# Performance work log

Hardware: AMD Instinct MI355X
Metric: run time of the kernel (lower is better)

## Reference

```python
import jax, jax.numpy as jnp
import numpy as np

N_E = 8192      # codebook size
E_DIM = 256     # codebook dim
BETA = 0.25

def setup_inputs() -> dict:
    key = jax.random.key(0)
    k1, k2 = jax.random.split(key)
    z = jax.random.normal(k1, (4, E_DIM, 16, 16, 16), dtype=jnp.float32)
    weight = jax.random.normal(k2, (N_E, E_DIM), dtype=jnp.float32)
    return {"z": z, "weight": weight}

def reference(z, weight):
    # b c d h w -> b d h w c
    z_t = jnp.transpose(z, (0, 2, 3, 4, 1))
    zf = z_t.reshape(-1, E_DIM)                          # [N, e_dim]
    # l2 pairwise distances: |z|^2 + |w|^2 - 2 z.w^T
    d = (jnp.sum(zf * zf, axis=1, keepdims=True)
         + jnp.sum(weight * weight, axis=1)
         - 2.0 * jnp.einsum('bd,nd->bn', zf, weight))    # [N, n_e]
    idx = jnp.argmin(d, axis=1)                          # [N]
    z_q = weight[idx].reshape(z_t.shape)                 # gather lookup
    # perplexity from cluster assignment histogram (avoids dense one-hot)
    counts = jax.ops.segment_sum(jnp.ones_like(idx, dtype=z.dtype), idx,
                                 num_segments=N_E)
    avg_probs = counts / zf.shape[0]
    perplexity = jnp.exp(-jnp.sum(avg_probs * jnp.log(avg_probs + 1e-10)))
    # commitment loss (z_q detached)
    loss = BETA * jnp.mean((jax.lax.stop_gradient(z_q) - z_t) ** 2)
    # straight-through estimator
    z_q_st = z_t + jax.lax.stop_gradient(z_q - z_t)
    out = jnp.transpose(z_q_st, (0, 4, 1, 2, 3))         # b d h w c -> b c d h w
    return out, loss, perplexity, idx
```

## Files before the change

kernel.cpp:

```cpp
#include <hip/hip_runtime.h>
#include <stdint.h>


#define M_TOTAL 16384
#define N_CODES 8192
#define KDIM    256
#define SPATIAL 4096
#define NSPLIT  8
#define CODES_PER_SPLIT  1024
#define CHUNK_CODES      16
#define CHUNKS_PER_SPLIT 64
#define CHUNK_BYTES      9216
#define CHUNK_HALFS      4608

typedef _Float16 v8hf __attribute__((ext_vector_type(8)));
typedef _Float16 v4hf __attribute__((ext_vector_type(4)));
typedef float    v4f  __attribute__((ext_vector_type(4)));

#define WAITCNT_VM9   0x0F79
#define WAITCNT_VM0   0x0F70
#define WAITCNT_LGKM0 0xC07F

__global__ __launch_bounds__(256) void prep_w_kernel(
    const float* __restrict__ w, _Float16* __restrict__ wpk,
    int* __restrict__ counts, double* __restrict__ loss_acc)
{
    const int t = threadIdx.x;
    const int n = blockIdx.x * 4 + (t >> 6);
    const int lane = t & 63;
    v4f v = ((const v4f*)(w + (size_t)n * KDIM))[lane];
    v4hf hv;
    float s = 0.0f;
#pragma unroll
    for (int j = 0; j < 4; j++) {
        float f = v[j];
        s += f * f;
        hv[j] = (_Float16)f;
    }
    const int chunk = n >> 4;
    const int row   = n & 15;
    const int g     = lane >> 1;
    const int gg    = g ^ (n & 7);
    size_t off = (size_t)chunk * CHUNK_HALFS + row * 256 + gg * 8 + (lane & 1) * 4;
    *(v4hf*)(wpk + off) = hv;
#pragma unroll
    for (int o = 32; o >= 1; o >>= 1) s += __shfl_xor(s, o);
    if (lane == 0) {
        float* hwp = (float*)((char*)wpk + (size_t)chunk * CHUNK_BYTES + 8192);
        hwp[row] = 1024.0f - 0.5f * s;
    }
    const int gi = blockIdx.x * 256 + t;
    if (gi < N_CODES) counts[gi] = 0;
    if (gi == 0) *loss_acc = 0.0;
}

__device__ __forceinline__ void top2max_merge(uint32_t& v1, int& i1, uint32_t& v2, int& i2,
                                              uint32_t o1, int oi1, uint32_t o2, int oi2) {
    bool ob = (o1 > v1) || (o1 == v1 && oi1 < i1);
    uint32_t n1v, n2v; int n1i, n2i;
    if (ob) {
        bool t2 = (v1 > o2) || (v1 == o2 && i1 < oi2);
        n1v = o1; n1i = oi1;
        n2v = t2 ? v1 : o2; n2i = t2 ? i1 : oi2;
    } else {
        bool t2 = (o1 > v2) || (o1 == v2 && oi1 < i2);
        n1v = v1; n1i = i1;
        n2v = t2 ? o1 : v2; n2i = t2 ? oi1 : i2;
    }
    v1 = n1v; i1 = n1i; v2 = n2v; i2 = n2i;
}

__global__ __launch_bounds__(64, 2) void gemm_kernel(
    const float* __restrict__ z,
    const _Float16* __restrict__ wpk,
    int4* __restrict__ candbuf)
{
    __shared__ __align__(16) _Float16 lds[2][CHUNK_HALFS];

    const int bid   = blockIdx.x;
    const int split = bid & 7;
    const int rb    = bid >> 3;
    const int i0    = rb * 64;
    const int b     = i0 >> 12;
    const int s0    = i0 & (SPATIAL - 1);
    const int lane  = threadIdx.x;
    const int r     = lane & 15;
    const int q     = lane >> 4;

    const char* wsplit = (const char*)wpk + (size_t)split * CHUNKS_PER_SPLIT * CHUNK_BYTES;
    auto stage = [&](int chunk, int buf) {
        const char* gb = wsplit + (size_t)chunk * CHUNK_BYTES + lane * 16;
        _Float16* lb = &lds[buf][lane * 8];
#pragma unroll
        for (int j = 0; j < 9; j++) {
            __builtin_amdgcn_global_load_lds(
                (const __attribute__((address_space(1))) void*)(gb + j * 1024),
                (__attribute__((address_space(3))) void*)(lb + j * 512), 16, 0, 0);
        }
    };
    stage(0, 0);
    stage(1, 1);

    v8hf a[4][8];
    {
        const float* zb = z + ((size_t)b << 20) + (size_t)(s0 + r);
#pragma unroll
        for (int mt = 0; mt < 4; mt++) {
#pragma unroll
            for (int ks = 0; ks < 8; ks++) {
                const int kbase = ks * 32 + q * 8;
#pragma unroll
                for (int j = 0; j < 8; j++)
                    a[mt][ks][j] = (_Float16)zb[((size_t)(kbase + j) << 12) + mt * 16];
            }
        }
    }

    uint32_t k1[4][4], k2[4][4];
#pragma unroll
    for (int mt = 0; mt < 4; mt++)
#pragma unroll
    for (int g = 0; g < 4; g++) { k1[mt][g] = 0u; k2[mt][g] = 0u; }

    const int swz = r & 7;

    auto body = [&](int it, int buf) {
        const float hwv = *(const float*)((const char*)&lds[buf][0] + 8192 + r * 4);
        v4f acc[4];
#pragma unroll
        for (int mt = 0; mt < 4; mt++) acc[mt] = (v4f){hwv, hwv, hwv, hwv};

        const _Float16* L = &lds[buf][0];
#pragma unroll
        for (int ks = 0; ks < 8; ks++) {
            const int gran = ((ks << 2) | q) ^ swz;
            v8hf bh = *(const v8hf*)(L + r * 256 + (gran << 3));
#pragma unroll
            for (int mt = 0; mt < 4; mt++)
                acc[mt] = __builtin_amdgcn_mfma_f32_16x16x32_f16(a[mt][ks], bh, acc[mt], 0, 0, 0);
        }
        const uint32_t tag = (uint32_t)it;
#pragma unroll
        for (int mt = 0; mt < 4; mt++)
#pragma unroll
        for (int g = 0; g < 4; g++) {
            uint32_t key = (__float_as_uint(acc[mt][g]) & 0xFFFFFFC0u) | tag;
            uint32_t o1 = k1[mt][g], o2 = k2[mt][g];
            uint32_t hi = key > o2 ? key : o2;
            k2[mt][g] = hi < o1 ? hi : o1;
            k1[mt][g] = key > o1 ? key : o1;
        }
    };

#pragma unroll 1
    for (int it = 0; it < CHUNKS_PER_SPLIT - 1; it++) {
        const int buf = it & 1;
        __builtin_amdgcn_s_waitcnt(WAITCNT_VM9);
        body(it, buf);
        __builtin_amdgcn_s_waitcnt(WAITCNT_LGKM0);
        if (it < CHUNKS_PER_SPLIT - 2) stage(it + 2, buf);
    }
    __builtin_amdgcn_s_waitcnt(WAITCNT_VM0);
    body(CHUNKS_PER_SPLIT - 1, (CHUNKS_PER_SPLIT - 1) & 1);

    const int nsbase = split * CODES_PER_SPLIT + r;
#pragma unroll
    for (int mt = 0; mt < 4; mt++) {
#pragma unroll
        for (int g = 0; g < 4; g++) {
            uint32_t K1 = k1[mt][g], K2 = k2[mt][g];
            int n1 = nsbase + (int)((K1 & 63u) << 4);
            int n2 = nsbase + (int)((K2 & 63u) << 4);
#pragma unroll
            for (int off = 1; off < 16; off <<= 1) {
                uint32_t o1 = __shfl_xor(K1, off);
                int     on1 = __shfl_xor(n1, off);
                uint32_t o2 = __shfl_xor(K2, off);
                int     on2 = __shfl_xor(n2, off);
                top2max_merge(K1, n1, K2, n2, o1, on1, o2, on2);
            }
            if (r == 0) {
                const int row = i0 + mt * 16 + q * 4 + g;
                candbuf[(size_t)row * 8 + split] = make_int4((int)K1, n1, (int)K2, n2);
            }
        }
    }
}

__global__ __launch_bounds__(256) void finish_kernel(
    const float* __restrict__ z, const float* __restrict__ weight,
    const int4* __restrict__ candbuf,
    int* __restrict__ counts, double* __restrict__ loss_acc,
    float* __restrict__ out, float* __restrict__ out_idx_f)
{
    __shared__ int4  s_cand[32][8];
    __shared__ float s_zw[32][KDIM + 1];
    __shared__ int   s_fi[32];
    __shared__ double s_loss[4];

    const int i0 = blockIdx.x * 32;
    const int b  = i0 >> 12;
    const int s0 = i0 & (SPATIAL - 1);
    const int t  = threadIdx.x;

    s_cand[t >> 3][t & 7] = candbuf[(size_t)(i0 + (t >> 3)) * 8 + (t & 7)];

    for (int e = t; e < 32 * KDIM; e += 256) {
        const int c = e >> 5, rr = e & 31;
        s_zw[rr][c] = z[((size_t)b << 20) + ((size_t)c << 12) + s0 + rr];
    }
    __syncthreads();

    const int row = t >> 3, seg = t & 7;
    float zs[32];
#pragma unroll
    for (int j = 0; j < 32; j++) zs[j] = s_zw[row][seg * 32 + j];

    float da[16];
    float dmin_a = 3.4e38f;
#pragma unroll
    for (int sp = 0; sp < 8; sp++) {
        int4 c = s_cand[row][sp];
        da[sp * 2]     = 2048.0f - 2.0f * __uint_as_float((uint32_t)c.x & 0xFFFFFFC0u);
        da[sp * 2 + 1] = 2048.0f - 2.0f * __uint_as_float((uint32_t)c.z & 0xFFFFFFC0u);
        dmin_a = fminf(dmin_a, fminf(da[sp * 2], da[sp * 2 + 1]));
    }
    const float cutoff = dmin_a + 0.5f;

    double dbest = 1e300; int nbest = 0x7fffffff;
#pragma unroll 1
    for (int c = 0; c < 16; c++) {
        if (da[c] > cutoff) continue;
        int4 cc = s_cand[row][c >> 1];
        const int n = (c & 1) ? cc.w : cc.y;
        const float* wr = weight + (size_t)n * KDIM + seg * 32;
        double d = 0.0;
#pragma unroll
        for (int j = 0; j < 32; j++) {
            double df = (double)zs[j] - (double)wr[j];
            d += df * df;
        }
#pragma unroll
        for (int o = 1; o < 8; o <<= 1) d += __shfl_xor(d, o);
        if (d < dbest || (d == dbest && n < nbest)) { dbest = d; nbest = n; }
    }

    double lsum = 0.0;
    if (seg == 0) {
        s_fi[row] = nbest;
        out_idx_f[i0 + row] = (float)nbest;
        atomicAdd(&counts[nbest], 1);
        lsum = dbest;
    }
#pragma unroll
    for (int o = 1; o < 64; o <<= 1) lsum += __shfl_xor(lsum, o);
    if ((t & 63) == 0) s_loss[t >> 6] = lsum;
    __syncthreads();
    if (t == 0) atomicAdd(loss_acc, s_loss[0] + s_loss[1] + s_loss[2] + s_loss[3]);

    for (int e = t; e < 32 * KDIM; e += 256) {
        const int rr = e >> 8, c = e & 255;
        s_zw[rr][c] = weight[(size_t)s_fi[rr] * KDIM + c];
    }
    __syncthreads();
    const int m = t & 31, c0 = t >> 5;
    const size_t obase = ((size_t)b << 20) + (size_t)(s0 + m);
    for (int c = c0; c < KDIM; c += 8)
        out[obase + ((size_t)c << 12)] = s_zw[m][c];
}

__global__ void finalize_kernel(const int* __restrict__ counts,
                                const double* __restrict__ loss_acc,
                                float* __restrict__ out_scalars)
{
    const int t = threadIdx.x;
    double s = 0.0;
    for (int n = t; n < N_CODES; n += 256) {
        double p = (double)counts[n] / (double)M_TOTAL;
        s -= p * log(p + 1e-10);
    }
#pragma unroll
    for (int o = 32; o >= 1; o >>= 1) s += __shfl_xor(s, o);
    __shared__ double sds[4];
    if ((t & 63) == 0) sds[t >> 6] = s;
    __syncthreads();
    if (t == 0) {
        double tot = sds[0] + sds[1] + sds[2] + sds[3];
        out_scalars[0] = (float)(0.25 * (*loss_acc) / (double)(M_TOTAL * KDIM));
        out_scalars[1] = (float)exp(tot);
    }
}

extern "C" void kernel_launch(void* const* d_in, const int* in_sizes, int n_in,
                              void* d_out, int out_size, void* d_ws, size_t ws_size,
                              hipStream_t stream) {
    const float* z      = (const float*)d_in[0];
    const float* weight = (const float*)d_in[1];
    float* out = (float*)d_out;

    size_t off = 0;
    auto carve = [&](size_t bytes) {
        void* p = (char*)d_ws + off;
        off += (bytes + 255) & ~(size_t)255;
        return p;
    };
    _Float16* wpk     = (_Float16*)carve((size_t)(N_CODES / CHUNK_CODES) * CHUNK_BYTES);
    int4*     candbuf = (int4*)    carve((size_t)M_TOTAL * 8 * 16);
    int*      counts  = (int*)     carve((size_t)N_CODES * 4);
    double*   lossac  = (double*)  carve(16);

    float* out_scalars = out + (size_t)4 * KDIM * SPATIAL;
    float* out_idx_f   = out_scalars + 2;

    prep_w_kernel<<<dim3(N_CODES / 4), dim3(256), 0, stream>>>(weight, wpk, counts, lossac);
    gemm_kernel<<<dim3(M_TOTAL / 64 * NSPLIT), dim3(64), 0, stream>>>(z, wpk, candbuf);
    finish_kernel<<<dim3(M_TOTAL / 32), dim3(256), 0, stream>>>(
        z, weight, candbuf, counts, lossac, out, out_idx_f);
    finalize_kernel<<<dim3(1), dim3(256), 0, stream>>>(counts, lossac, out_scalars);
}
```

Baseline: 212.5 us.

## Share codebook LDS tiles across four waves per block with barrier-synced staging

The GEMM block grows from one wave (64 rows) to four waves (256 rows) that share each staged codebook chunk in LDS. This cuts redundant global-to-LDS weight traffic by a factor of four. The packed weight layout is changed so each lane reads its B fragment with a contiguous lane-indexed load, with no XOR swizzle. Barriers are added around the double-buffered stages, and s_setprio is raised around the MFMA loop. The cost is block-wide synchronization each iteration and fewer, larger blocks.

```diff
diff --git a/kernel.cpp b/kernel.cpp
--- a/kernel.cpp
+++ b/kernel.cpp
@@ -12,12 +12,13 @@
 #define CHUNKS_PER_SPLIT 64
 #define CHUNK_BYTES      9216
 #define CHUNK_HALFS      4608
+#define M_BLOCK          256
 
 typedef _Float16 v8hf __attribute__((ext_vector_type(8)));
 typedef _Float16 v4hf __attribute__((ext_vector_type(4)));
 typedef float    v4f  __attribute__((ext_vector_type(4)));
 
-#define WAITCNT_VM9   0x0F79
+#define WAITCNT_VM3   0x0F73
 #define WAITCNT_VM0   0x0F70
 #define WAITCNT_LGKM0 0xC07F
 
@@ -39,9 +40,10 @@
     }
     const int chunk = n >> 4;
     const int row   = n & 15;
-    const int g     = lane >> 1;
-    const int gg    = g ^ (n & 7);
-    size_t off = (size_t)chunk * CHUNK_HALFS + row * 256 + gg * 8 + (lane & 1) * 4;
+    const int ks = lane >> 3;
+    const int qq = (lane >> 1) & 3;
+    const int hh = lane & 1;
+    size_t off = (size_t)chunk * CHUNK_HALFS + ks * 512 + qq * 128 + row * 8 + hh * 4;
     *(v4hf*)(wpk + off) = hv;
 #pragma unroll
     for (int o = 32; o >= 1; o >>= 1) s += __shfl_xor(s, o);
@@ -70,7 +72,7 @@
     v1 = n1v; i1 = n1i; v2 = n2v; i2 = n2i;
 }
 
-__global__ __launch_bounds__(64, 2) void gemm_kernel(
+__global__ __launch_bounds__(256, 2) void gemm_kernel(
     const float* __restrict__ z,
     const _Float16* __restrict__ wpk,
     int4* __restrict__ candbuf)
@@ -80,30 +82,39 @@
     const int bid   = blockIdx.x;
     const int split = bid & 7;
     const int rb    = bid >> 3;
-    const int i0    = rb * 64;
+    const int i0    = rb * M_BLOCK;
     const int b     = i0 >> 12;
     const int s0    = i0 & (SPATIAL - 1);
-    const int lane  = threadIdx.x;
+    const int tid   = threadIdx.x;
+    const int wid   = tid >> 6;
+    const int lane  = tid & 63;
     const int r     = lane & 15;
     const int q     = lane >> 4;
 
     const char* wsplit = (const char*)wpk + (size_t)split * CHUNKS_PER_SPLIT * CHUNK_BYTES;
-    auto stage = [&](int chunk, int buf) {
-        const char* gb = wsplit + (size_t)chunk * CHUNK_BYTES + lane * 16;
-        _Float16* lb = &lds[buf][lane * 8];
-#pragma unroll
-        for (int j = 0; j < 9; j++) {
+
+    auto stage = [&](int c, int buf) {
+        const char* gb = wsplit + (size_t)c * CHUNK_BYTES;
+        char* lb = (char*)&lds[buf][0];
+#pragma unroll
+        for (int j = 0; j < 2; j++) {
+            const int o = (wid * 2 + j) * 1024 + lane * 16;
             __builtin_amdgcn_global_load_lds(
-                (const __attribute__((address_space(1))) void*)(gb + j * 1024),
-                (__attribute__((address_space(3))) void*)(lb + j * 512), 16, 0, 0);
-        }
+                (const __attribute__((address_space(1))) void*)(gb + o),
+                (__attribute__((address_space(3))) void*)(lb + o), 16, 0, 0);
+        }
+        const int oh = 8192 + wid * 256 + lane * 4;
+        __builtin_amdgcn_global_load_lds(
+            (const __attribute__((address_space(1))) void*)(gb + oh),
+            (__attribute__((address_space(3))) void*)(lb + oh), 4, 0, 0);
     };
+
     stage(0, 0);
     stage(1, 1);
 
     v8hf a[4][8];
     {
-        const float* zb = z + ((size_t)b << 20) + (size_t)(s0 + r);
+        const float* zb = z + ((size_t)b << 20) + (size_t)(s0 + wid * 64 + r);
 #pragma unroll
         for (int mt = 0; mt < 4; mt++) {
 #pragma unroll
@@ -122,23 +133,23 @@
 #pragma unroll
     for (int g = 0; g < 4; g++) { k1[mt][g] = 0u; k2[mt][g] = 0u; }
 
-    const int swz = r & 7;
-
-    auto body = [&](int it, int buf) {
-        const float hwv = *(const float*)((const char*)&lds[buf][0] + 8192 + r * 4);
+    auto compute = [&](int it, int buf) {
+        const char* lb = (const char*)&lds[buf][0];
+        const float hwv = *(const float*)(lb + 8192 + r * 4);
         v4f acc[4];
 #pragma unroll
         for (int mt = 0; mt < 4; mt++) acc[mt] = (v4f){hwv, hwv, hwv, hwv};
 
-        const _Float16* L = &lds[buf][0];
+        __builtin_amdgcn_s_setprio(1);
 #pragma unroll
         for (int ks = 0; ks < 8; ks++) {
-            const int gran = ((ks << 2) | q) ^ swz;
-            v8hf bh = *(const v8hf*)(L + r * 256 + (gran << 3));
+            v8hf bh = *(const v8hf*)(lb + ks * 1024 + lane * 16);
 #pragma unroll
             for (int mt = 0; mt < 4; mt++)
                 acc[mt] = __builtin_amdgcn_mfma_f32_16x16x32_f16(a[mt][ks], bh, acc[mt], 0, 0, 0);
         }
+        __builtin_amdgcn_s_setprio(0);
+
         const uint32_t tag = (uint32_t)it;
 #pragma unroll
         for (int mt = 0; mt < 4; mt++)
@@ -146,22 +157,31 @@
         for (int g = 0; g < 4; g++) {
             uint32_t key = (__float_as_uint(acc[mt][g]) & 0xFFFFFFC0u) | tag;
             uint32_t o1 = k1[mt][g], o2 = k2[mt][g];
-            uint32_t hi = key > o2 ? key : o2;
-            k2[mt][g] = hi < o1 ? hi : o1;
+            uint32_t mn = key < o1 ? key : o1;
+            k2[mt][g] = o2 > mn ? o2 : mn;
             k1[mt][g] = key > o1 ? key : o1;
         }
     };
 
-#pragma unroll 1
-    for (int it = 0; it < CHUNKS_PER_SPLIT - 1; it++) {
+    __builtin_amdgcn_s_waitcnt(WAITCNT_VM0);
+    __builtin_amdgcn_s_barrier();
+
+#pragma unroll 2
+    for (int it = 0; it < CHUNKS_PER_SPLIT - 2; it++) {
         const int buf = it & 1;
-        __builtin_amdgcn_s_waitcnt(WAITCNT_VM9);
-        body(it, buf);
+        __builtin_amdgcn_s_waitcnt(WAITCNT_VM3);
+        __builtin_amdgcn_s_barrier();
+        compute(it, buf);
         __builtin_amdgcn_s_waitcnt(WAITCNT_LGKM0);
-        if (it < CHUNKS_PER_SPLIT - 2) stage(it + 2, buf);
-    }
+        __builtin_amdgcn_s_barrier();
+        stage(it + 2, buf);
+    }
+    __builtin_amdgcn_s_waitcnt(WAITCNT_VM3);
+    __builtin_amdgcn_s_barrier();
+    compute(CHUNKS_PER_SPLIT - 2, 0);
     __builtin_amdgcn_s_waitcnt(WAITCNT_VM0);
-    body(CHUNKS_PER_SPLIT - 1, (CHUNKS_PER_SPLIT - 1) & 1);
+    __builtin_amdgcn_s_barrier();
+    compute(CHUNKS_PER_SPLIT - 1, 1);
 
     const int nsbase = split * CODES_PER_SPLIT + r;
 #pragma unroll
@@ -180,7 +200,7 @@
                 top2max_merge(K1, n1, K2, n2, o1, on1, o2, on2);
             }
             if (r == 0) {
-                const int row = i0 + mt * 16 + q * 4 + g;
+                const int row = i0 + wid * 64 + mt * 16 + q * 4 + g;
                 candbuf[(size_t)row * 8 + split] = make_int4((int)K1, n1, (int)K2, n2);
             }
         }
@@ -313,7 +333,7 @@
     float* out_idx_f   = out_scalars + 2;
 
     prep_w_kernel<<<dim3(N_CODES / 4), dim3(256), 0, stream>>>(weight, wpk, counts, lossac);
-    gemm_kernel<<<dim3(M_TOTAL / 64 * NSPLIT), dim3(64), 0, stream>>>(z, wpk, candbuf);
+    gemm_kernel<<<dim3(M_TOTAL / M_BLOCK * NSPLIT), dim3(256), 0, stream>>>(z, wpk, candbuf);
     finish_kernel<<<dim3(M_TOTAL / 32), dim3(256), 0, stream>>>(
         z, weight, candbuf, counts, lossac, out, out_idx_f);
     finalize_kernel<<<dim3(1), dim3(256), 0, stream>>>(counts, lossac, out_scalars);
```

Result: faster. 192.0 us (-9.7%).
